# Performance work log

Hardware: AMD Instinct MI355X
Metric: run time of the kernel (lower is better)

The kernel has to match this reference:

```python
import jax, jax.numpy as jnp
import numpy as np
from jax import lax

B, C, H, W = 8, 64, 64, 64
C8 = C // 8
EPS = 1e-5


def setup_inputs() -> dict:
    key = jax.random.key(0)
    ks = jax.random.split(key, 10)
    s = lambda *sh: 0.02
    inp = {
        "x": jax.random.normal(ks[0], (B, C, H, W), dtype=jnp.float32),
        "conv_b_w": jax.random.normal(ks[1], (C8, C), dtype=jnp.float32) * 0.05,
        "conv_b_b": jnp.zeros((C8,), jnp.float32),
        "conv_c_w": jax.random.normal(ks[2], (C8, C), dtype=jnp.float32) * 0.05,
        "conv_c_b": jnp.zeros((C8,), jnp.float32),
        "conv_d_w": jax.random.normal(ks[3], (C, C), dtype=jnp.float32) * 0.05,
        "conv_d_b": jnp.zeros((C,), jnp.float32),
        "alpha": jnp.zeros((1,), jnp.float32) + 0.1,  # learned PAM scale
        "beta": jnp.zeros((1,), jnp.float32) + 0.1,   # learned CAM scale
        "conv_w": jax.random.normal(ks[4], (2 * C, C, 3, 3), dtype=jnp.float32) * 0.02,
        "conv_bias": jnp.zeros((2 * C,), jnp.float32),
        "bn_gamma": jnp.ones((2 * C,), jnp.float32),
        "bn_beta": jnp.zeros((2 * C,), jnp.float32),
    }
    return inp


def _conv1x1(x, w, b):
    # x: [B,C,H,W], w: [O,C] -> [B,O,H,W]
    return jnp.einsum('oc,bchw->bohw', w, x) + b[None, :, None, None]


def _forward(x, conv_b_w, conv_b_b, conv_c_w, conv_c_b, conv_d_w, conv_d_b,
             alpha, beta, conv_w, conv_bias, bn_gamma, bn_beta):
    b, c, h, w = x.shape
    n = h * w
    # ---- Position Attention Module ----
    feat_b = _conv1x1(x, conv_b_w, conv_b_b).reshape(b, C8, n)   # [B,C8,N]
    feat_c = _conv1x1(x, conv_c_w, conv_c_b).reshape(b, C8, n)   # [B,C8,N]
    # torch: bmm(feat_b^T [B,N,C8], feat_c [B,C8,N]) -> [B,N,N]
    attn_s = jax.nn.softmax(jnp.einsum('bcn,bcm->bnm', feat_b, feat_c), axis=-1)
    feat_d = _conv1x1(x, conv_d_w, conv_d_b).reshape(b, c, n)    # [B,C,N]
    # torch: bmm(feat_d, attn_s^T) -> out[b,c,n] = sum_m feat_d[b,c,m]*attn[b,n,m]
    feat_e = jnp.einsum('bcm,bnm->bcn', feat_d, attn_s).reshape(b, c, h, w)
    x = alpha[0] * feat_e + x
    # ---- Channel Attention Module ----
    fa = x.reshape(b, c, n)                                      # [B,C,N]
    att = jnp.einsum('bcn,bdn->bcd', fa, fa)                     # [B,C,C]
    att_new = jnp.max(att, axis=-1, keepdims=True) - att
    att = jax.nn.softmax(att_new, axis=-1)
    fe = jnp.einsum('bcd,bdn->bcn', att, fa).reshape(b, c, h, w)
    x = beta[0] * fe + x
    # ---- conv3x3 + BN (batch stats) + ReLU + maxpool(2,2,pad=(1,0)) ----
    out = lax.conv_general_dilated(x, conv_w, (1, 1), ((1, 1), (1, 1)),
                                   dimension_numbers=('NCHW', 'OIHW', 'NCHW'))
    out = out + conv_bias[None, :, None, None]
    mean = jnp.mean(out, axis=(0, 2, 3), keepdims=True)
    var = jnp.var(out, axis=(0, 2, 3), keepdims=True)
    out = (out - mean) * lax.rsqrt(var + EPS)
    out = out * bn_gamma[None, :, None, None] + bn_beta[None, :, None, None]
    out = jax.nn.relu(out)
    # MaxPool2d(kernel=2, stride=2, padding=(1,0)): -inf padding on height only
    out = lax.reduce_window(out, -jnp.inf, lax.max,
                            (1, 1, 2, 2), (1, 1, 2, 2),
                            ((0, 0), (0, 0), (1, 1), (0, 0)))
    return out


def reference(x, conv_b_w, conv_b_b, conv_c_w, conv_c_b, conv_d_w, conv_d_b,
              alpha, beta, conv_w, conv_bias, bn_gamma, bn_beta):
    return _forward(x, conv_b_w, conv_b_b, conv_c_w, conv_c_b, conv_d_w, conv_d_b,
                    alpha, beta, conv_w, conv_bias, bn_gamma, bn_beta)
```

## Files before the change

kernel.cpp:

```cpp
#include <hip/hip_runtime.h>

using f32x4  = __attribute__((ext_vector_type(4))) float;
using f32x16 = __attribute__((ext_vector_type(16))) float;
using bf16x8 = __attribute__((ext_vector_type(8))) short;
using u32x4  = __attribute__((ext_vector_type(4))) unsigned int;
using u32x2  = __attribute__((ext_vector_type(2))) unsigned int;
typedef unsigned short u16;

__device__ __forceinline__ u16 f2bf(float f) {
  unsigned u = __float_as_uint(f);
  unsigned r = (u + 0x7FFFu + ((u >> 16) & 1u)) >> 16;
  return (u16)r;
}

#if __has_builtin(__builtin_amdgcn_exp2f)
#define FAST_EXP2(x) __builtin_amdgcn_exp2f(x)
#else
#define FAST_EXP2(x) __expf(0.6931471805599453f * (x))
#endif

#define LOG2E 1.4426950408889634f

__device__ __forceinline__ void permswap32(unsigned& a, unsigned& b) {
  asm volatile("v_permlane32_swap_b32 %0, %1" : "+v"(a), "+v"(b));
}

__global__ void __launch_bounds__(256) k1_conv1x1(
    const float* __restrict__ x, const float* __restrict__ wB, const float* __restrict__ bB,
    const float* __restrict__ wC, const float* __restrict__ bC,
    const float* __restrict__ wD, const float* __restrict__ bD,
    u16* __restrict__ featBb, u16* __restrict__ featCb, u16* __restrict__ featD,
    const float* __restrict__ cw, u16* __restrict__ wb) {
  const int t = threadIdx.x;
  const int b = blockIdx.y;
  const int z = blockIdx.z;
  if (z == 3) {
    int gid = (b * 16 + blockIdx.x) * 256 + t;
#pragma unroll
    for (int k = 0; k < 3; ++k) {
      int F = gid + k * 32768;
      if (F < 73728) {
        int j = F & 7, lane = (F >> 3) & 63, T = F >> 9;
        int tap = T >> 4, g = (T >> 1) & 7, kc = T & 1;
        int l16 = lane & 15, quad = lane >> 4;
        int oc = g * 16 + l16, ic = kc * 32 + quad * 8 + j;
        wb[F] = f2bf(cw[(oc * 64 + ic) * 9 + tap]);
      }
    }
    return;
  }
  __shared__ float W[2048];
  __shared__ float Bias[32];
  const int n = blockIdx.x * 256 + t;
  if (z == 0) {
    for (int i = t; i < 512; i += 256) W[i] = wB[i];
    for (int i = t; i < 512; i += 256) W[512 + i] = wC[i];
    if (t < 8) Bias[t] = bB[t];
    if (t >= 8 && t < 16) Bias[t] = bC[t - 8];
  } else {
    const float* wsrc = wD + (z - 1) * 2048;
    for (int i = t; i < 2048; i += 256) W[i] = wsrc[i];
    if (t < 32) Bias[t] = bD[(z - 1) * 32 + t];
  }
  __syncthreads();
  float xv[64];
#pragma unroll
  for (int c = 0; c < 64; ++c) xv[c] = x[((b * 64 + c) << 12) + n];
  if (z == 0) {
    float o[16];
#pragma unroll
    for (int k = 0; k < 16; ++k) {
      f32x4 s = {0.f, 0.f, 0.f, 0.f};
#pragma unroll
      for (int cq = 0; cq < 16; ++cq) {
        f32x4 wv = *(const f32x4*)&W[k * 64 + cq * 4];
        f32x4 xq = {xv[cq * 4], xv[cq * 4 + 1], xv[cq * 4 + 2], xv[cq * 4 + 3]};
        s += wv * xq;
      }
      o[k] = Bias[k] + s[0] + s[1] + s[2] + s[3];
    }
    int base = ((b << 12) + n) * 8;
    u32x4 pb, pc;
#pragma unroll
    for (int i = 0; i < 4; ++i) {
      pb[i] = (unsigned)f2bf(o[2 * i] * LOG2E) | ((unsigned)f2bf(o[2 * i + 1] * LOG2E) << 16);
      pc[i] = (unsigned)f2bf(o[8 + 2 * i]) | ((unsigned)f2bf(o[8 + 2 * i + 1]) << 16);
    }
    *(u32x4*)&featBb[base] = pb;
    *(u32x4*)&featCb[base] = pc;
  } else {
#pragma unroll 4
    for (int k = 0; k < 32; ++k) {
      f32x4 s = {0.f, 0.f, 0.f, 0.f};
#pragma unroll
      for (int cq = 0; cq < 16; ++cq) {
        f32x4 wv = *(const f32x4*)&W[k * 64 + cq * 4];
        f32x4 xq = {xv[cq * 4], xv[cq * 4 + 1], xv[cq * 4 + 2], xv[cq * 4 + 3]};
        s += wv * xq;
      }
      float val = Bias[k] + s[0] + s[1] + s[2] + s[3];
      featD[((b * 64 + (z - 1) * 32 + k) << 12) + n] = f2bf(val);
    }
  }
}

__global__ void __launch_bounds__(256) k2_pam_part(
    const u16* __restrict__ fBb, const u16* __restrict__ fCb, const u16* __restrict__ fD,
    u16* __restrict__ numPart, float* __restrict__ denPart) {
  __shared__ u16 Df[2][64 * 132];
  const int t = threadIdx.x, b = blockIdx.y, z = blockIdx.z;
  const int w = t >> 6, lane = t & 63, l32 = lane & 31, hi = lane >> 5;
  const int nb = blockIdx.x * 128 + w * 32;
  const int mz = z << 10;

  int srow[4], smo[4];
#pragma unroll
  for (int hh = 0; hh < 4; ++hh) {
    int idx = hh * 256 + t;
    srow[hh] = idx >> 4;
    smo[hh] = (idx & 15) << 3;
  }

  bf16x8 bq = (bf16x8)(short)0;
  if (hi == 0) bq = *(const bf16x8*)&fBb[(((b << 12) + nb + l32) << 3)];

  bf16x8 onesA = (bf16x8)(short)0;
  if (l32 == 0) onesA = (bf16x8)(short)0x3F80;

  f32x16 acc0 = (f32x16)(0.0f), acc1 = (f32x16)(0.0f), accd = (f32x16)(0.0f);

  u32x4 sreg[4];
#define K2_ISSUE(CH) {                                                        \
    int m0_ = mz + ((CH) << 7);                                               \
    _Pragma("unroll")                                                         \
    for (int hh = 0; hh < 4; ++hh)                                            \
      sreg[hh] = *(const u32x4*)&fD[((b * 64 + srow[hh]) << 12) + m0_ + smo[hh]]; }
#define K2_WRITE(BUF) {                                                       \
    _Pragma("unroll")                                                         \
    for (int hh = 0; hh < 4; ++hh)                                            \
      *(u32x4*)&Df[BUF][srow[hh] * 132 + smo[hh]] = sreg[hh]; }

  K2_ISSUE(0);
  K2_WRITE(0);
  __syncthreads();

#pragma unroll 2
  for (int ch = 0; ch < 8; ++ch) {
    const int cur = ch & 1;
    const int m0 = mz + (ch << 7);
    if (ch < 7) K2_ISSUE(ch + 1);

    bf16x8 afv[4];
#pragma unroll
    for (int mt2 = 0; mt2 < 4; ++mt2) {
      bf16x8 a = (bf16x8)(short)0;
      if (hi == 0) a = *(const bf16x8*)&fCb[(((b << 12) + m0 + mt2 * 32 + l32) << 3)];
      afv[mt2] = a;
    }

#pragma unroll
    for (int mt2 = 0; mt2 < 4; ++mt2) {
      f32x16 s = __builtin_amdgcn_mfma_f32_32x32x16_bf16(afv[mt2], bq, (f32x16)(0.0f), 0, 0, 0);
      unsigned u0[8];
#pragma unroll
      for (int i = 0; i < 8; ++i) {
        float e0 = FAST_EXP2(s[2 * i]);
        float e1 = FAST_EXP2(s[2 * i + 1]);
        u0[i] = __builtin_amdgcn_perm(__float_as_uint(e1), __float_as_uint(e0), 0x07060302u);
      }
      permswap32(u0[0], u0[2]); permswap32(u0[1], u0[3]);
      permswap32(u0[4], u0[6]); permswap32(u0[5], u0[7]);

#pragma unroll
      for (int kc = 0; kc < 2; ++kc) {
        u32x4 q0 = {u0[4 * kc], u0[4 * kc + 1], u0[4 * kc + 2], u0[4 * kc + 3]};
        bf16x8 bv0 = *(bf16x8*)&q0;
        bf16x8 av0 = *(const bf16x8*)&Df[cur][(l32) * 132 + mt2 * 32 + kc * 16 + hi * 8];
        bf16x8 av1 = *(const bf16x8*)&Df[cur][(32 + l32) * 132 + mt2 * 32 + kc * 16 + hi * 8];
        acc0 = __builtin_amdgcn_mfma_f32_32x32x16_bf16(av0, bv0, acc0, 0, 0, 0);
        acc1 = __builtin_amdgcn_mfma_f32_32x32x16_bf16(av1, bv0, acc1, 0, 0, 0);
        accd = __builtin_amdgcn_mfma_f32_32x32x16_bf16(onesA, bv0, accd, 0, 0, 0);
      }
    }

    if (ch < 7) K2_WRITE(cur ^ 1);
    __syncthreads();
  }
#undef K2_ISSUE
#undef K2_WRITE

  const int zb = z * 8 + b;
#pragma unroll
  for (int r = 0; r < 16; ++r) {
    int c = (r & 3) + ((r >> 2) << 3) + (hi << 2);
    numPart[((zb * 64 + c) << 12) + nb + l32] = (u16)(__float_as_uint(acc0[r]) >> 16);
    numPart[((zb * 64 + c + 32) << 12) + nb + l32] = (u16)(__float_as_uint(acc1[r]) >> 16);
  }
  if (hi == 0) denPart[(zb << 12) + nb + l32] = accd[0];
}

__global__ void __launch_bounds__(256) k3_gram(
    const u16* __restrict__ numPart, const float* __restrict__ denPart,
    const float* __restrict__ x, const float* __restrict__ alpha,
    float* __restrict__ x1, float* __restrict__ attPart) {
  __shared__ float X[64 * 132];
  __shared__ float Dinv[128];
  const int t = threadIdx.x, b = blockIdx.y, cx = blockIdx.x;
  const int n0 = cx * 128;
  if (t < 128) {
    float den = 0.f;
#pragma unroll
    for (int z = 0; z < 4; ++z) den += denPart[(((z * 8 + b) << 12)) + n0 + t];
    Dinv[t] = alpha[0] / den;
  }
  __syncthreads();
  for (int idx = t; idx < 4096; idx += 256) {
    int row = idx >> 6, cp = (idx & 63) * 2;
    int gi = ((b * 64 + row) << 12) + n0 + cp;
    float num0 = 0.f, num1 = 0.f;
#pragma unroll
    for (int z = 0; z < 4; ++z) {
      unsigned v = *(const unsigned*)&numPart[(((z * 8 + b) * 64 + row) << 12) + n0 + cp];
      num0 += __uint_as_float(v << 16);
      num1 += __uint_as_float(v & 0xFFFF0000u);
    }
    float v0 = num0 * Dinv[cp] + x[gi];
    float v1 = num1 * Dinv[cp + 1] + x[gi + 1];
    X[row * 132 + cp] = v0;
    X[row * 132 + cp + 1] = v1;
    x1[gi] = v0;
    x1[gi + 1] = v1;
  }
  __syncthreads();
  const int cg = t >> 4, dg = t & 15;
  f32x4 acc[4][4];
#pragma unroll
  for (int i = 0; i < 4; ++i)
#pragma unroll
    for (int k = 0; k < 4; ++k) acc[i][k] = (f32x4){0.f, 0.f, 0.f, 0.f};
  for (int nq0 = 0; nq0 < 32; ++nq0) {
    int nq = (nq0 + dg) & 31;
    f32x4 a[4], bb[4];
#pragma unroll
    for (int i = 0; i < 4; ++i) a[i] = *(const f32x4*)&X[(cg * 4 + i) * 132 + nq * 4];
#pragma unroll
    for (int k = 0; k < 4; ++k) bb[k] = *(const f32x4*)&X[(dg * 4 + k) * 132 + nq * 4];
#pragma unroll
    for (int i = 0; i < 4; ++i)
#pragma unroll
      for (int k = 0; k < 4; ++k) acc[i][k] += a[i] * bb[k];
  }
#pragma unroll
  for (int i = 0; i < 4; ++i)
#pragma unroll
    for (int k = 0; k < 4; ++k) {
      f32x4 s = acc[i][k];
      attPart[((b * 32 + cx) * 64 + cg * 4 + i) * 64 + dg * 4 + k] = s[0] + s[1] + s[2] + s[3];
    }
}

__global__ void __launch_bounds__(256) k4_softmax(const float* __restrict__ attPart, float* __restrict__ attP) {
  const int b = blockIdx.y, t = threadIdx.x;
  const int c = (blockIdx.x << 2) + (t >> 6), d = t & 63;
  float v = 0.f;
  for (int p = 0; p < 32; ++p) v += attPart[((b * 32 + p) * 64 + c) * 64 + d];
  float mn = v;
#pragma unroll
  for (int off = 1; off < 64; off <<= 1) mn = fminf(mn, __shfl_xor(mn, off));
  float e = __expf(mn - v);
  float sum = e;
#pragma unroll
  for (int off = 1; off < 64; off <<= 1) sum += __shfl_xor(sum, off);
  attP[(b * 64 + c) * 64 + d] = e / sum;
}

__global__ void __launch_bounds__(256) k5_apply(
    const float* __restrict__ attP, const float* __restrict__ x1,
    const float* __restrict__ beta, u16* __restrict__ x2b) {
  __shared__ float A[64 * 68];
  const int t = threadIdx.x, b = blockIdx.y;
  for (int idx = t; idx < 4096; idx += 256) A[(idx >> 6) * 68 + (idx & 63)] = attP[(b << 12) + idx];
  __syncthreads();
  const int n = blockIdx.x * 64 + (t & 63);
  const int cq = t >> 6;
  const float bv = beta[0];
  float acc[16];
#pragma unroll
  for (int i = 0; i < 16; ++i) acc[i] = 0.f;
  const float* xcol = x1 + ((size_t)b << 18) + n;
#pragma unroll 4
  for (int dq = 0; dq < 16; ++dq) {
    float x0 = xcol[(size_t)(dq * 4 + 0) << 12];
    float x1v = xcol[(size_t)(dq * 4 + 1) << 12];
    float x2 = xcol[(size_t)(dq * 4 + 2) << 12];
    float x3 = xcol[(size_t)(dq * 4 + 3) << 12];
#pragma unroll
    for (int i = 0; i < 16; ++i) {
      const float* av = &A[(cq * 16 + i) * 68 + dq * 4];
      acc[i] += av[0] * x0 + av[1] * x1v + av[2] * x2 + av[3] * x3;
    }
  }
  u16* orow = x2b + ((((size_t)(b << 12) + n) << 6) + cq * 16);
  unsigned pk[8];
#pragma unroll
  for (int i = 0; i < 16; i += 2) {
    float v0 = bv * acc[i] + xcol[(size_t)(cq * 16 + i) << 12];
    float v1 = bv * acc[i + 1] + xcol[(size_t)(cq * 16 + i + 1) << 12];
    pk[i >> 1] = (unsigned)f2bf(v0) | ((unsigned)f2bf(v1) << 16);
  }
  *(u32x4*)&orow[0] = *(u32x4*)&pk[0];
  *(u32x4*)&orow[8] = *(u32x4*)&pk[4];
}

__global__ void __launch_bounds__(256) k6_mfma(const u16* __restrict__ x2b, const u16* __restrict__ wb,
                                               float* __restrict__ y) {
  __shared__ u16 Xl[3 * 66 * 72];
  const int t = threadIdx.x, b = blockIdx.y, h = blockIdx.x;
  for (int idx = t; idx < 3 * 66 * 8; idx += 256) {
    int r = idx / 528;
    int rem = idx - r * 528;
    int c = rem >> 3, icq = rem & 7;
    int gy = h - 1 + r, gx = c - 1;
    u32x4 v = {0u, 0u, 0u, 0u};
    if (gy >= 0 && gy < 64 && gx >= 0 && gx < 64)
      v = *(const u32x4*)&x2b[(((size_t)(b << 6 | gy) << 6) + gx) * 64 + icq * 8];
    *(u32x4*)&Xl[(r * 66 + c) * 72 + icq * 8] = v;
  }
  __syncthreads();
  const int w = t >> 6, lane = t & 63, quad = lane >> 4, l16 = lane & 15;
  const int mBase = (w & 1) * 64;
  const int og = (w & 1) * 4;
  const int nBase = (w >> 1) * 32;
  f32x4 acc[4][2];
#pragma unroll
  for (int ot = 0; ot < 4; ++ot)
#pragma unroll
    for (int nt = 0; nt < 2; ++nt) acc[ot][nt] = (f32x4){0.f, 0.f, 0.f, 0.f};
#pragma unroll 3
  for (int tap = 0; tap < 9; ++tap) {
    const int dy = tap / 3, dx = tap - dy * 3;
    bf16x8 af[4][2];
#pragma unroll
    for (int ot = 0; ot < 4; ++ot)
#pragma unroll
      for (int kc = 0; kc < 2; ++kc)
        af[ot][kc] = *(const bf16x8*)&wb[((((tap * 8 + og + ot) * 2 + kc) << 6) + lane) << 3];
#pragma unroll
    for (int nt = 0; nt < 2; ++nt) {
      const int prow = dy * 66 + nBase + nt * 16 + l16 + dx;
#pragma unroll
      for (int kc = 0; kc < 2; ++kc) {
        bf16x8 bv = *(const bf16x8*)&Xl[prow * 72 + kc * 32 + quad * 8];
#pragma unroll
        for (int ot = 0; ot < 4; ++ot)
          acc[ot][nt] = __builtin_amdgcn_mfma_f32_16x16x32_bf16(af[ot][kc], bv, acc[ot][nt], 0, 0, 0);
      }
    }
  }
#pragma unroll
  for (int ot = 0; ot < 4; ++ot)
#pragma unroll
    for (int nt = 0; nt < 2; ++nt)
#pragma unroll
      for (int r = 0; r < 4; ++r) {
        int oc = mBase + ot * 16 + quad * 4 + r;
        int pix = nBase + nt * 16 + l16;
        y[((b * 128 + oc) << 12) + (h << 6) + pix] = acc[ot][nt][r];
      }
}

__global__ void __launch_bounds__(256) k7_part(const float* __restrict__ y, float* __restrict__ pstats) {
  const int ch = blockIdx.x, q = blockIdx.y, t = threadIdx.x;
  float s = 0.f, ss = 0.f;
#pragma unroll
  for (int bb = 0; bb < 2; ++bb) {
    const float* p = y + (((q * 2 + bb) * 128 + ch) << 12);
#pragma unroll
    for (int i = 0; i < 16; ++i) { float v = p[i * 256 + t]; s += v; ss += v * v; }
  }
#pragma unroll
  for (int off = 1; off < 64; off <<= 1) { s += __shfl_xor(s, off); ss += __shfl_xor(ss, off); }
  __shared__ float rs[4], rss[4];
  if ((t & 63) == 0) { rs[t >> 6] = s; rss[t >> 6] = ss; }
  __syncthreads();
  if (t == 0) {
    pstats[ch * 8 + q * 2]     = rs[0] + rs[1] + rs[2] + rs[3];
    pstats[ch * 8 + q * 2 + 1] = rss[0] + rss[1] + rss[2] + rss[3];
  }
}

__global__ void __launch_bounds__(256) k8_pool(const float* __restrict__ y, const float* __restrict__ pstats,
                                               const float* __restrict__ gamma, const float* __restrict__ bbeta,
                                               float* __restrict__ out) {
  const int bc = blockIdx.x;
  const int ch = bc & 127;
  float S = 0.f, SS = 0.f;
#pragma unroll
  for (int q = 0; q < 4; ++q) { S += pstats[ch * 8 + q * 2]; SS += pstats[ch * 8 + q * 2 + 1]; }
  const float mean = S * (1.f / 32768.f);
  const float var = SS * (1.f / 32768.f) - mean * mean;
  const float sc = gamma[ch] * rsqrtf(var + 1e-5f);
  const float sh = bbeta[ch] - mean * sc;
  const float* p = y + (bc << 12);
  float* op = out + bc * (33 * 32);
  for (int i = threadIdx.x; i < 33 * 32; i += 256) {
    int oh = i >> 5, ow = i & 31;
    int r0 = 2 * oh - 1, r1 = 2 * oh;
    float m = 0.f;
    if (r0 >= 0) {
      m = fmaxf(m, p[r0 * 64 + 2 * ow] * sc + sh);
      m = fmaxf(m, p[r0 * 64 + 2 * ow + 1] * sc + sh);
    }
    if (r1 <= 63) {
      m = fmaxf(m, p[r1 * 64 + 2 * ow] * sc + sh);
      m = fmaxf(m, p[r1 * 64 + 2 * ow + 1] * sc + sh);
    }
    op[i] = m;
  }
}

extern "C" void kernel_launch(void* const* d_in, const int* in_sizes, int n_in,
                              void* d_out, int out_size, void* d_ws, size_t ws_size,
                              hipStream_t stream) {
  const float* x      = (const float*)d_in[0];
  const float* wB     = (const float*)d_in[1];
  const float* bB     = (const float*)d_in[2];
  const float* wC     = (const float*)d_in[3];
  const float* bC     = (const float*)d_in[4];
  const float* wD     = (const float*)d_in[5];
  const float* bD     = (const float*)d_in[6];
  const float* alpha  = (const float*)d_in[7];
  const float* beta   = (const float*)d_in[8];
  const float* cw     = (const float*)d_in[9];
  const float* gamma  = (const float*)d_in[11];
  const float* bnbeta = (const float*)d_in[12];

  char* ws = (char*)d_ws;
  u16*   featBb  = (u16*)  (ws + 0);
  u16*   featCb  = (u16*)  (ws + 524288);
  u16*   fDb     = (u16*)  (ws + 1048576);
  u16*   x2b     = (u16*)  (ws + 0);
  float* x1      = (float*)(ws + 5242880);
  u16*   numPart = (u16*)  (ws + 13631488);
  float* y       = (float*)(ws + 13631488);
  float* denPart = (float*)(ws + 30408704);
  float* attPart = (float*)(ws + 30932992);
  float* attP    = (float*)(ws + 35127296);
  u16*   wb      = (u16*)  (ws + 35258368);
  float* pstats  = (float*)(ws + 35405824);
  float* outp    = (float*)d_out;

  k1_conv1x1<<<dim3(16, 8, 4), 256, 0, stream>>>(x, wB, bB, wC, bC, wD, bD, featBb, featCb, fDb, cw, wb);
  k2_pam_part<<<dim3(32, 8, 4), 256, 0, stream>>>(featBb, featCb, fDb, numPart, denPart);
  k3_gram<<<dim3(32, 8), 256, 0, stream>>>(numPart, denPart, x, alpha, x1, attPart);
  k4_softmax<<<dim3(16, 8), 256, 0, stream>>>(attPart, attP);
  k5_apply<<<dim3(64, 8), 256, 0, stream>>>(attP, x1, beta, x2b);
  k6_mfma<<<dim3(64, 8), 256, 0, stream>>>(x2b, wb, y);
  k7_part<<<dim3(128, 4), 256, 0, stream>>>(y, pstats);
  k8_pool<<<dim3(1024), 256, 0, stream>>>(y, pstats, gamma, bnbeta, outp);
}
```

Before: 184.0 us.

## Fuse BN partial statistics into conv epilogue and software-pipeline PAM score MFMAs

The conv3x3 MFMA kernel now reduces per-channel sum and sum-of-squares from its accumulators through shuffles and LDS, then writes per-block partials. This removes the separate stats kernel and its full reread of y. The pool kernel now reduces 512 partials per channel instead of 4, which adds a little work to every block. In the PAM kernel, the score MFMA for the next tile is issued before the exp of the current tile, and the accumulate MFMAs are raised to high priority with s_setprio, so matrix work and transcendental work can overlap.

```diff
diff --git a/kernel.cpp b/kernel.cpp
--- a/kernel.cpp
+++ b/kernel.cpp
@@ -158,19 +158,22 @@
       afv[mt2] = a;
     }
 
+    f32x16 sc = __builtin_amdgcn_mfma_f32_32x32x16_bf16(afv[0], bq, (f32x16)(0.0f), 0, 0, 0);
 #pragma unroll
     for (int mt2 = 0; mt2 < 4; ++mt2) {
-      f32x16 s = __builtin_amdgcn_mfma_f32_32x32x16_bf16(afv[mt2], bq, (f32x16)(0.0f), 0, 0, 0);
+      f32x16 sn;
+      if (mt2 < 3) sn = __builtin_amdgcn_mfma_f32_32x32x16_bf16(afv[mt2 + 1], bq, (f32x16)(0.0f), 0, 0, 0);
       unsigned u0[8];
 #pragma unroll
       for (int i = 0; i < 8; ++i) {
-        float e0 = FAST_EXP2(s[2 * i]);
-        float e1 = FAST_EXP2(s[2 * i + 1]);
+        float e0 = FAST_EXP2(sc[2 * i]);
+        float e1 = FAST_EXP2(sc[2 * i + 1]);
         u0[i] = __builtin_amdgcn_perm(__float_as_uint(e1), __float_as_uint(e0), 0x07060302u);
       }
       permswap32(u0[0], u0[2]); permswap32(u0[1], u0[3]);
       permswap32(u0[4], u0[6]); permswap32(u0[5], u0[7]);
 
+      __builtin_amdgcn_s_setprio(1);
 #pragma unroll
       for (int kc = 0; kc < 2; ++kc) {
         u32x4 q0 = {u0[4 * kc], u0[4 * kc + 1], u0[4 * kc + 2], u0[4 * kc + 3]};
@@ -181,6 +184,8 @@
         acc1 = __builtin_amdgcn_mfma_f32_32x32x16_bf16(av1, bv0, acc1, 0, 0, 0);
         accd = __builtin_amdgcn_mfma_f32_32x32x16_bf16(onesA, bv0, accd, 0, 0, 0);
       }
+      __builtin_amdgcn_s_setprio(0);
+      if (mt2 < 3) sc = sn;
     }
 
     if (ch < 7) K2_WRITE(cur ^ 1);
@@ -313,8 +318,9 @@
 }
 
 __global__ void __launch_bounds__(256) k6_mfma(const u16* __restrict__ x2b, const u16* __restrict__ wb,
-                                               float* __restrict__ y) {
+                                               float* __restrict__ y, float* __restrict__ pstat2) {
   __shared__ u16 Xl[3 * 66 * 72];
+  __shared__ float pp[4][64][2];
   const int t = threadIdx.x, b = blockIdx.y, h = blockIdx.x;
   for (int idx = t; idx < 3 * 66 * 8; idx += 256) {
     int r = idx / 528;
@@ -367,36 +373,61 @@
         int pix = nBase + nt * 16 + l16;
         y[((b * 128 + oc) << 12) + (h << 6) + pix] = acc[ot][nt][r];
       }
-}
-
-__global__ void __launch_bounds__(256) k7_part(const float* __restrict__ y, float* __restrict__ pstats) {
-  const int ch = blockIdx.x, q = blockIdx.y, t = threadIdx.x;
-  float s = 0.f, ss = 0.f;
-#pragma unroll
-  for (int bb = 0; bb < 2; ++bb) {
-    const float* p = y + (((q * 2 + bb) * 128 + ch) << 12);
-#pragma unroll
-    for (int i = 0; i < 16; ++i) { float v = p[i * 256 + t]; s += v; ss += v * v; }
-  }
-#pragma unroll
-  for (int off = 1; off < 64; off <<= 1) { s += __shfl_xor(s, off); ss += __shfl_xor(ss, off); }
-  __shared__ float rs[4], rss[4];
-  if ((t & 63) == 0) { rs[t >> 6] = s; rss[t >> 6] = ss; }
-  __syncthreads();
-  if (t == 0) {
-    pstats[ch * 8 + q * 2]     = rs[0] + rs[1] + rs[2] + rs[3];
-    pstats[ch * 8 + q * 2 + 1] = rss[0] + rss[1] + rss[2] + rss[3];
-  }
-}
-
-__global__ void __launch_bounds__(256) k8_pool(const float* __restrict__ y, const float* __restrict__ pstats,
+  float bs[4][4], bss[4][4];
+#pragma unroll
+  for (int ot = 0; ot < 4; ++ot)
+#pragma unroll
+    for (int r = 0; r < 4; ++r) {
+      float v0 = acc[ot][0][r], v1 = acc[ot][1][r];
+      bs[ot][r] = v0 + v1;
+      bss[ot][r] = v0 * v0 + v1 * v1;
+    }
+#pragma unroll
+  for (int off = 1; off < 16; off <<= 1) {
+#pragma unroll
+    for (int ot = 0; ot < 4; ++ot)
+#pragma unroll
+      for (int r = 0; r < 4; ++r) {
+        bs[ot][r] += __shfl_xor(bs[ot][r], off);
+        bss[ot][r] += __shfl_xor(bss[ot][r], off);
+      }
+  }
+  if (l16 == 0) {
+#pragma unroll
+    for (int ot = 0; ot < 4; ++ot)
+#pragma unroll
+      for (int r = 0; r < 4; ++r) {
+        int ocl = ot * 16 + quad * 4 + r;
+        pp[w][ocl][0] = bs[ot][r];
+        pp[w][ocl][1] = bss[ot][r];
+      }
+  }
+  __syncthreads();
+  {
+    int oc = t >> 1, st = t & 1;
+    float v = (oc < 64) ? (pp[0][oc][st] + pp[2][oc][st])
+                        : (pp[1][oc - 64][st] + pp[3][oc - 64][st]);
+    pstat2[(oc * 2 + st) * 512 + (b << 6) + h] = v;
+  }
+}
+
+__global__ void __launch_bounds__(256) k8_pool(const float* __restrict__ y, const float* __restrict__ pstat2,
                                                const float* __restrict__ gamma, const float* __restrict__ bbeta,
                                                float* __restrict__ out) {
   const int bc = blockIdx.x;
   const int ch = bc & 127;
-  float S = 0.f, SS = 0.f;
-#pragma unroll
-  for (int q = 0; q < 4; ++q) { S += pstats[ch * 8 + q * 2]; SS += pstats[ch * 8 + q * 2 + 1]; }
+  float s = 0.f, ss = 0.f;
+  for (int i = threadIdx.x; i < 512; i += 256) {
+    s += pstat2[ch * 1024 + i];
+    ss += pstat2[ch * 1024 + 512 + i];
+  }
+#pragma unroll
+  for (int off = 1; off < 64; off <<= 1) { s += __shfl_xor(s, off); ss += __shfl_xor(ss, off); }
+  __shared__ float rs[4], rss[4];
+  if ((threadIdx.x & 63) == 0) { rs[threadIdx.x >> 6] = s; rss[threadIdx.x >> 6] = ss; }
+  __syncthreads();
+  const float S = rs[0] + rs[1] + rs[2] + rs[3];
+  const float SS = rss[0] + rss[1] + rss[2] + rss[3];
   const float mean = S * (1.f / 32768.f);
   const float var = SS * (1.f / 32768.f) - mean * mean;
   const float sc = gamma[ch] * rsqrtf(var + 1e-5f);
@@ -445,9 +476,9 @@
   float* y       = (float*)(ws + 13631488);
   float* denPart = (float*)(ws + 30408704);
   float* attPart = (float*)(ws + 30932992);
+  float* pstat2  = (float*)(ws + 30932992);
   float* attP    = (float*)(ws + 35127296);
   u16*   wb      = (u16*)  (ws + 35258368);
-  float* pstats  = (float*)(ws + 35405824);
   float* outp    = (float*)d_out;
 
   k1_conv1x1<<<dim3(16, 8, 4), 256, 0, stream>>>(x, wB, bB, wC, bC, wD, bD, featBb, featCb, fDb, cw, wb);
@@ -455,7 +486,6 @@
   k3_gram<<<dim3(32, 8), 256, 0, stream>>>(numPart, denPart, x, alpha, x1, attPart);
   k4_softmax<<<dim3(16, 8), 256, 0, stream>>>(attPart, attP);
   k5_apply<<<dim3(64, 8), 256, 0, stream>>>(attP, x1, beta, x2b);
-  k6_mfma<<<dim3(64, 8), 256, 0, stream>>>(x2b, wb, y);
-  k7_part<<<dim3(128, 4), 256, 0, stream>>>(y, pstats);
-  k8_pool<<<dim3(1024), 256, 0, stream>>>(y, pstats, gamma, bnbeta, outp);
-}
+  k6_mfma<<<dim3(64, 8), 256, 0, stream>>>(x2b, wb, y, pstat2);
+  k8_pool<<<dim3(1024), 256, 0, stream>>>(y, pstat2, gamma, bnbeta, outp);
+}
```

Result: no change. 184.0 us (-0.0%).
